# Kernel optimization log

Hardware: AMD Instinct MI355X
Metric: run time of the kernel (lower is better)

The kernel has to match this reference:

```python
import jax, jax.numpy as jnp
import numpy as np
import math

B, S, HID, NH = 2, 2048, 1024, 16
HD = HID // NH


def setup_inputs() -> dict:
    key = jax.random.key(0)
    ks = jax.random.split(key, 6)
    scale = 0.02
    return {
        "hidden_states": jax.random.normal(ks[0], (B, S, HID), dtype=jnp.float32),
        "attention_mask": jnp.ones((B, S), dtype=jnp.float32),
        "Wq": jax.random.normal(ks[1], (HID, HID), dtype=jnp.float32) * scale,
        "bq": jnp.zeros((HID,), dtype=jnp.float32),
        "Wk": jax.random.normal(ks[2], (HID, HID), dtype=jnp.float32) * scale,
        "bk": jnp.zeros((HID,), dtype=jnp.float32),
        "Wv": jax.random.normal(ks[3], (HID, HID), dtype=jnp.float32) * scale,
        "bv": jnp.zeros((HID,), dtype=jnp.float32),
        "Wo": jax.random.normal(ks[4], (HID, HID), dtype=jnp.float32) * scale,
        "bo": jnp.zeros((HID,), dtype=jnp.float32),
        "beta": jnp.zeros((1,), dtype=jnp.float32),
        "gamma": jnp.ones((1,), dtype=jnp.float32),
    }


def reference(hidden_states, attention_mask, Wq, bq, Wk, bk, Wv, bv, Wo, bo, beta, gamma):
    b, s, h = hidden_states.shape

    def proj(W, bias):
        # torch Linear: x @ W.T + b ; then split heads -> [B, NH, S, HD]
        y = jnp.einsum('bsh,oh->bso', hidden_states, W) + bias
        return y.reshape(b, s, NH, HD).transpose(0, 2, 1, 3)

    q = proj(Wq, bq)
    k = proj(Wk, bk)
    v = proj(Wv, bv)

    scores = jnp.einsum('bnsd,bntd->bnst', q, k) / math.sqrt(HD)  # [B,NH,S,S]
    # extended mask: [B,1,1,S]; additive -1e4 on masked positions
    scores = scores + (1.0 - attention_mask)[:, None, None, :] * (-10000.0)

    # ConsMax: exp(scores - beta - rowmax) / gamma (no sum normalization)
    shifted = scores - beta
    shifted = shifted - jnp.max(shifted, axis=-1, keepdims=True)
    probs = jnp.exp(shifted) / gamma  # dropout p=0 -> identity

    ctx = jnp.einsum('bnst,bntd->bnsd', probs, v)  # [B,NH,S,HD]
    ctx = ctx.transpose(0, 2, 1, 3).reshape(b, s, h)
    return jnp.einsum('bsh,oh->bso', ctx, Wo) + bo
```

## Files before the change

### kernel.cpp

```cpp
#include <hip/hip_runtime.h>
#include <hip/hip_bf16.h>


typedef unsigned short u16;
typedef __attribute__((ext_vector_type(8))) short short8;
typedef __attribute__((ext_vector_type(4))) float floatx4;
typedef __attribute__((ext_vector_type(16))) float floatx16;

constexpr int B_  = 2;
constexpr int S_  = 2048;
constexpr int HID = 1024;
constexpr int NH  = 16;
constexpr int HD  = 64;

constexpr float LOG2E   = 1.4426950408889634f;
constexpr float QSCALE  = 0.125f * LOG2E;
constexpr float MSCALE  = -10000.0f * LOG2E;

#if __has_builtin(__builtin_amdgcn_exp2f)
#define EXP2(x) __builtin_amdgcn_exp2f(x)
#else
#define EXP2(x) exp2f(x)
#endif

__device__ __forceinline__ u16 f2us(float f) {
    union { float f; unsigned int i; } x;
    x.f = f;
    unsigned int r = x.i + 0x7FFFu + ((x.i >> 16) & 1u);
    return (u16)(r >> 16);
}
__device__ __forceinline__ unsigned pk2(float a, float b) {
    __hip_bfloat162 h = __float22bfloat162_rn(make_float2(a, b));
    unsigned u; __builtin_memcpy(&u, &h, 4); return u;
}
__device__ __forceinline__ void async_lds16(const u16* g, u16* l) {
    __builtin_amdgcn_global_load_lds(
        (const __attribute__((address_space(1))) unsigned int*)g,
        (__attribute__((address_space(3))) unsigned int*)l, 16, 0, 0);
}

__global__ __launch_bounds__(256)
void cvt_all(const float* __restrict__ hs, const float* __restrict__ Wq,
             const float* __restrict__ Wk, const float* __restrict__ Wv,
             const float* __restrict__ Wo,
             u16* __restrict__ hs_bf, u16* __restrict__ Wcat,
             u16* __restrict__ Wo_bf)
{
    const int bid = blockIdx.x;
    const float* src;
    u16* dst;
    size_t base;
    if (bid < 4096) {
        src = hs; dst = hs_bf; base = (size_t)bid * 1024;
    } else if (bid < 7168) {
        const int s = (bid - 4096) >> 10;
        src = (s == 0) ? Wq : (s == 1) ? Wk : Wv;
        dst = Wcat + (size_t)s * 1048576;
        base = (size_t)((bid - 4096) & 1023) * 1024;
    } else {
        src = Wo; dst = Wo_bf; base = (size_t)(bid - 7168) * 1024;
    }
    const size_t i = base + threadIdx.x * 4;
    float4 t = *(const float4*)(src + i);
    uint2 o = { pk2(t.x, t.y), pk2(t.z, t.w) };
    *(uint2*)(dst + i) = o;
}

__global__ __launch_bounds__(256)
void qkv_gemm(const u16* __restrict__ hs_bf, const u16* __restrict__ Wcat,
              const float* __restrict__ bq, const float* __restrict__ bk,
              const float* __restrict__ bv,
              u16* __restrict__ Qo, u16* __restrict__ Ko, u16* __restrict__ VT)
{
    __shared__ u16 Alds[3][4096];
    __shared__ u16 Blds[3][4096];

    const int tid = threadIdx.x;
    const int id  = blockIdx.x;
    const int xcd = id & 7, jb = id >> 3;
    const int m0  = (xcd * 4 + (jb & 3)) * 128;
    const int n0g = (jb >> 2) * 128;
    const int p   = n0g >> 10;
    const int n0  = n0g & 1023;
    const u16*   Wb = Wcat + (size_t)p * 1048576;
    const float* bi = (p == 0) ? bq : (p == 1) ? bk : bv;
    const float  osc = (p == 0) ? QSCALE : 1.0f;

    const int w = tid >> 6, l = tid & 63;
    const int quad = l >> 4, l16 = l & 15;
    const int wy = w >> 1, wx = w & 1;

    floatx4 acc[4][4];
    #pragma unroll
    for (int i = 0; i < 4; ++i)
        #pragma unroll
        for (int j = 0; j < 4; ++j) acc[i][j] = (floatx4){0.f, 0.f, 0.f, 0.f};

    auto stage = [&](int ks, int bf) {
        const int k0 = ks * 32;
        #pragma unroll
        for (int c = 0; c < 2; ++c) {
            const int s = w * 2 + c;
            async_lds16(hs_bf + (size_t)(m0 + s * 16 + l16) * HID + k0 + quad * 8,
                        &Alds[bf][s * 512]);
            async_lds16(Wb + (size_t)(n0 + s * 16 + l16) * HID + k0 + quad * 8,
                        &Blds[bf][s * 512]);
        }
    };

    constexpr int NS = HID / 32;
    stage(0, 0);
    stage(1, 1);

    for (int ks = 0; ks < NS; ++ks) {
        const int cur = ks % 3;
        if (ks < NS - 1) asm volatile("s_waitcnt vmcnt(4)" ::: "memory");
        else             asm volatile("s_waitcnt vmcnt(0)" ::: "memory");
        __builtin_amdgcn_s_barrier();
        if (ks + 2 < NS) stage(ks + 2, (ks + 2) % 3);

        short8 afr[4], bfr[4];
        #pragma unroll
        for (int i = 0; i < 4; ++i)
            afr[i] = *(const short8*)&Alds[cur][(wy * 4 + i) * 512 + l * 8];
        #pragma unroll
        for (int j = 0; j < 4; ++j)
            bfr[j] = *(const short8*)&Blds[cur][(wx * 4 + j) * 512 + l * 8];
        #pragma unroll
        for (int i = 0; i < 4; ++i)
            #pragma unroll
            for (int j = 0; j < 4; ++j)
                acc[i][j] = __builtin_amdgcn_mfma_f32_16x16x32_bf16(afr[i], bfr[j], acc[i][j], 0, 0, 0);
    }

    #pragma unroll
    for (int i = 0; i < 4; ++i)
        #pragma unroll
        for (int j = 0; j < 4; ++j) {
            const int nn   = n0 + wx * 64 + j * 16 + l16;
            const int head = nn >> 6, dd = nn & 63;
            const float bb_ = bi[nn];
            const int mmb = m0 + wy * 64 + i * 16 + quad * 4;
            const int b = mmb >> 11, ss = mmb & (S_ - 1);
            if (p == 2) {
                uint2 st = { pk2(acc[i][j][0] + bb_, acc[i][j][1] + bb_),
                             pk2(acc[i][j][2] + bb_, acc[i][j][3] + bb_) };
                *(uint2*)(VT + (((size_t)(b * NH + head)) * HD + dd) * S_ + ss) = st;
            } else {
                u16* Out = (p == 0) ? Qo : Ko;
                #pragma unroll
                for (int rg = 0; rg < 4; ++rg)
                    Out[(((size_t)b * NH + head) * S_ + ss + rg) * HD + dd] =
                        f2us((acc[i][j][rg] + bb_) * osc);
            }
        }
}

__global__ __launch_bounds__(512, 4)
void attn13(const u16* __restrict__ Qg, const u16* __restrict__ Kg,
            const u16* __restrict__ VTg, const float* __restrict__ mask,
            const float* __restrict__ gamma, u16* __restrict__ ctx)
{
    __shared__ u16 SMEM[36864];
    u16*   KbB = SMEM;
    u16*   VbB = SMEM + 12288;
    u16*   PqB = SMEM + 24576;
    float* Mb  = (float*)(SMEM + 32768);

    const int tid = threadIdx.x;
    const int w = tid >> 6, l = tid & 63;
    const int wq = w & 3, wk = w >> 2;
    const int l32 = l & 31, hh = l >> 5;
    const int swz = (l32 & 3) << 3;
    const int id  = blockIdx.x;
    const int xcd = id & 7, jb = id >> 3;
    const int bh  = xcd * 4 + (jb >> 4);
    const int qb  = jb & 15;
    const int b0  = bh >> 4, h = bh & (NH - 1);

    const u16* Qb    = Qg  + (size_t)bh * S_ * HD;
    const u16* Kbg   = Kg  + (size_t)bh * S_ * HD;
    const u16* Vbg   = VTg + (size_t)bh * HD * S_;
    const float* mG  = mask + (size_t)b0 * S_;

    const int qrow = qb * 128 + wq * 32 + l32;

    short8 qB[4];
    #pragma unroll
    for (int dc = 0; dc < 4; ++dc)
        qB[dc] = *(const short8*)(Qb + (size_t)qrow * HD + dc * 16 + hh * 8);

    {
        float4 mv = *(const float4*)(mG + tid * 4);
        float* d = &Mb[tid * 4];
        d[0] = fmaf(mv.x, -MSCALE, MSCALE);
        d[1] = fmaf(mv.y, -MSCALE, MSCALE);
        d[2] = fmaf(mv.z, -MSCALE, MSCALE);
        d[3] = fmaf(mv.w, -MSCALE, MSCALE);
    }

    floatx16 oacc[2];
    #pragma unroll
    for (int db = 0; db < 2; ++db)
        #pragma unroll
        for (int i = 0; i < 16; ++i) oacc[db][i] = 0.f;
    float m_run = -1e30f;

    u16* Kbuf = KbB + wk * 6144;
    u16* Vbuf = VbB + wk * 6144;
    u16* Pw   = PqB + w * 1024;

    auto stage = [&](int i, int bf) {
        const int kt = 2 * i + wk;
        async_lds16(Kbg + (size_t)(kt * 32 + l32) * HD + wq * 16 + hh * 8,
                    Kbuf + bf * 2048 + wq * 512);
        const int db = wq >> 1, kg = wq & 1;
        async_lds16(Vbg + (size_t)(db * 32 + l32) * S_ + kt * 32 + kg * 16 + hh * 8,
                    Vbuf + bf * 2048 + wq * 512);
    };

    __syncthreads();
    constexpr int NI = 32;
    stage(0, 0);
    stage(1, 1);

    for (int i = 0; i < NI; ++i) {
        const int cur = i % 3;
        if (i < NI - 1) asm volatile("s_waitcnt vmcnt(2)" ::: "memory");
        else            asm volatile("s_waitcnt vmcnt(0)" ::: "memory");
        __builtin_amdgcn_s_barrier();
        if (i + 2 < NI) stage(i + 2, (i + 2) % 3);

        const int kt = 2 * i + wk;

        const float* mrow = &Mb[kt * 32 + 4 * hh];
        floatx16 acc;
        #pragma unroll
        for (int g = 0; g < 4; ++g) {
            float4 mv = *(const float4*)(mrow + g * 8);
            acc[4*g]   = mv.x;
            acc[4*g+1] = mv.y;
            acc[4*g+2] = mv.z;
            acc[4*g+3] = mv.w;
        }
        #pragma unroll
        for (int dc = 0; dc < 4; ++dc) {
            short8 kf = *(const short8*)&Kbuf[cur * 2048 + dc * 512 + l * 8];
            acc = __builtin_amdgcn_mfma_f32_32x32x16_bf16(kf, qB[dc], acc, 0, 0, 0);
        }

        float mr = m_run;
        #pragma unroll
        for (int ii = 0; ii < 16; ++ii) mr = fmaxf(mr, acc[ii]);
        m_run = mr;
        #pragma unroll
        for (int g = 0; g < 4; ++g) {
            uint2 pw = { pk2(EXP2(acc[4*g]),   EXP2(acc[4*g+1])),
                         pk2(EXP2(acc[4*g+2]), EXP2(acc[4*g+3])) };
            const int koff = 8 * g + 4 * hh;
            *(uint2*)&Pw[l32 * 32 + (koff ^ swz)] = pw;
        }

        #pragma unroll
        for (int kg = 0; kg < 2; ++kg) {
            short8 pf = *(const short8*)&Pw[l32 * 32 + ((kg * 16 + hh * 8) ^ swz)];
            #pragma unroll
            for (int db = 0; db < 2; ++db) {
                short8 vf = *(const short8*)&Vbuf[cur * 2048 + (db * 2 + kg) * 512 + l * 8];
                oacc[db] = __builtin_amdgcn_mfma_f32_32x32x16_bf16(vf, pf, oacc[db], 0, 0, 0);
            }
        }
    }

    __syncthreads();
    float* OS = (float*)SMEM;
    if (wk == 1) {
        float* d = OS + (size_t)(wq * 64 + l) * 33;
        #pragma unroll
        for (int db = 0; db < 2; ++db)
            #pragma unroll
            for (int ii = 0; ii < 16; ++ii) d[db * 16 + ii] = oacc[db][ii];
        d[32] = m_run;
    }
    __syncthreads();
    if (wk == 0) {
        const float* s = OS + (size_t)(wq * 64 + l) * 33;
        #pragma unroll
        for (int db = 0; db < 2; ++db)
            #pragma unroll
            for (int ii = 0; ii < 16; ++ii) oacc[db][ii] += s[db * 16 + ii];
        m_run = fmaxf(m_run, s[32]);
        const float mx = fmaxf(m_run, __shfl_xor(m_run, 32, 64));
        const float si = EXP2(-mx) * (1.0f / gamma[0]);
        u16* crow = ctx + (size_t)(b0 * S_ + qrow) * HID + h * HD;
        #pragma unroll
        for (int db = 0; db < 2; ++db)
            #pragma unroll
            for (int g = 0; g < 4; ++g) {
                uint2 st = { pk2(oacc[db][g * 4 + 0] * si, oacc[db][g * 4 + 1] * si),
                             pk2(oacc[db][g * 4 + 2] * si, oacc[db][g * 4 + 3] * si) };
                *(uint2*)(crow + db * 32 + g * 8 + hh * 4) = st;
            }
    }
}

__global__ __launch_bounds__(256)
void out_gemm(const u16* __restrict__ ctx, const u16* __restrict__ Wo_bf,
              const float* __restrict__ bo, float* __restrict__ out)
{
    __shared__ u16 Alds[3][4096];
    __shared__ u16 Blds[3][2048];

    const int tid = threadIdx.x;
    const int id  = blockIdx.x;
    const int xcd = id & 7, jb = id >> 3;
    const int m0  = (xcd * 4 + (jb & 3)) * 128;
    const int n0  = (jb >> 2) * 64;

    const int w = tid >> 6, l = tid & 63;
    const int quad = l >> 4, l16 = l & 15;

    floatx4 acc[2][4];
    #pragma unroll
    for (int i = 0; i < 2; ++i)
        #pragma unroll
        for (int j = 0; j < 4; ++j) acc[i][j] = (floatx4){0.f, 0.f, 0.f, 0.f};

    auto stage = [&](int ks, int bf) {
        const int k0 = ks * 32;
        #pragma unroll
        for (int c = 0; c < 2; ++c) {
            const int s = w * 2 + c;
            async_lds16(ctx + (size_t)(m0 + s * 16 + l16) * HID + k0 + quad * 8,
                        &Alds[bf][s * 512]);
        }
        async_lds16(Wo_bf + (size_t)(n0 + w * 16 + l16) * HID + k0 + quad * 8,
                    &Blds[bf][w * 512]);
    };

    constexpr int NS = HID / 32;
    stage(0, 0);
    stage(1, 1);

    for (int ks = 0; ks < NS; ++ks) {
        const int cur = ks % 3;
        if (ks < NS - 1) asm volatile("s_waitcnt vmcnt(3)" ::: "memory");
        else             asm volatile("s_waitcnt vmcnt(0)" ::: "memory");
        __builtin_amdgcn_s_barrier();
        if (ks + 2 < NS) stage(ks + 2, (ks + 2) % 3);

        short8 afr[2], bfr[4];
        #pragma unroll
        for (int i = 0; i < 2; ++i)
            afr[i] = *(const short8*)&Alds[cur][(w * 2 + i) * 512 + l * 8];
        #pragma unroll
        for (int j = 0; j < 4; ++j)
            bfr[j] = *(const short8*)&Blds[cur][j * 512 + l * 8];
        #pragma unroll
        for (int i = 0; i < 2; ++i)
            #pragma unroll
            for (int j = 0; j < 4; ++j)
                acc[i][j] = __builtin_amdgcn_mfma_f32_16x16x32_bf16(afr[i], bfr[j], acc[i][j], 0, 0, 0);
    }

    #pragma unroll
    for (int i = 0; i < 2; ++i)
        #pragma unroll
        for (int j = 0; j < 4; ++j) {
            const int nn = n0 + j * 16 + l16;
            const float bb_ = bo[nn];
            #pragma unroll
            for (int rg = 0; rg < 4; ++rg) {
                const int mm = m0 + w * 32 + i * 16 + quad * 4 + rg;
                out[(size_t)mm * HID + nn] = acc[i][j][rg] + bb_;
            }
        }
}

extern "C" void kernel_launch(void* const* d_in, const int* in_sizes, int n_in,
                              void* d_out, int out_size, void* d_ws, size_t ws_size,
                              hipStream_t stream)
{
    const float* hs    = (const float*)d_in[0];
    const float* mask  = (const float*)d_in[1];
    const float* Wq    = (const float*)d_in[2];
    const float* bq    = (const float*)d_in[3];
    const float* Wk    = (const float*)d_in[4];
    const float* bk    = (const float*)d_in[5];
    const float* Wv    = (const float*)d_in[6];
    const float* bv    = (const float*)d_in[7];
    const float* Wo    = (const float*)d_in[8];
    const float* bo    = (const float*)d_in[9];
    const float* gamma = (const float*)d_in[11];
    float* out = (float*)d_out;

    const size_t tsz = (size_t)B_ * NH * S_ * HD;
    u16* q     = (u16*)d_ws;
    u16* vT    = q + tsz;
    u16* Wcat  = vT + tsz;
    u16* Wo_bf = Wcat + 3u * 1048576u;
    u16* ctx   = Wo_bf + 1048576u;
    u16* hs_bf = (u16*)d_out;
    u16* kbuf  = hs_bf + tsz;

    cvt_all<<<dim3(8192), 256, 0, stream>>>(hs, Wq, Wk, Wv, Wo, hs_bf, Wcat, Wo_bf);
    qkv_gemm<<<dim3(768), 256, 0, stream>>>(hs_bf, Wcat, bq, bk, bv, q, kbuf, vT);
    attn13<<<dim3(512), 512, 0, stream>>>(q, kbuf, vT, mask, gamma, ctx);
    out_gemm<<<dim3(512), 256, 0, stream>>>(ctx, Wo_bf, bo, out);
}
```

Baseline: 233.9 us.

## Load K/V directly into registers with double-buffered prefetch, dropping LDS staging

The attention kernel no longer stages K and V tiles through shared memory with async copies and per-iteration barriers. Each wave now loads its own K/V fragments straight from global memory into two register sets, alternating between them across 64-key tiles, which removes the block-wide barrier from the inner loop. The P tile is widened to 64 keys and its swizzle extended to match. The cost is far higher register pressure, since the launch-bounds occupancy hint was dropped and 32 short8 values are held live. Waves also stop sharing K/V loads, so global or L2 traffic rises.

After: 296.6 us. 1.27x slower.

```diff
diff --git a/kernel.cpp b/kernel.cpp
--- a/kernel.cpp
+++ b/kernel.cpp
@@ -156,22 +156,20 @@
         }
 }
 
-__global__ __launch_bounds__(512, 4)
-void attn13(const u16* __restrict__ Qg, const u16* __restrict__ Kg,
+__global__ __launch_bounds__(512)
+void attn14(const u16* __restrict__ Qg, const u16* __restrict__ Kg,
             const u16* __restrict__ VTg, const float* __restrict__ mask,
             const float* __restrict__ gamma, u16* __restrict__ ctx)
 {
-    __shared__ u16 SMEM[36864];
-    u16*   KbB = SMEM;
-    u16*   VbB = SMEM + 12288;
-    u16*   PqB = SMEM + 24576;
-    float* Mb  = (float*)(SMEM + 32768);
+    __shared__ u16 SMEM[20480];
+    u16*   PqB = SMEM;
+    float* Mb  = (float*)(SMEM + 16384);
 
     const int tid = threadIdx.x;
     const int w = tid >> 6, l = tid & 63;
     const int wq = w & 3, wk = w >> 2;
     const int l32 = l & 31, hh = l >> 5;
-    const int swz = (l32 & 3) << 3;
+    const int swz = (l32 & 7) << 3;
     const int id  = blockIdx.x;
     const int xcd = id & 7, jb = id >> 3;
     const int bh  = xcd * 4 + (jb >> 4);
@@ -198,6 +196,7 @@
         d[2] = fmaf(mv.z, -MSCALE, MSCALE);
         d[3] = fmaf(mv.w, -MSCALE, MSCALE);
     }
+    __syncthreads();
 
     floatx16 oacc[2];
     #pragma unroll
@@ -206,71 +205,65 @@
         for (int i = 0; i < 16; ++i) oacc[db][i] = 0.f;
     float m_run = -1e30f;
 
-    u16* Kbuf = KbB + wk * 6144;
-    u16* Vbuf = VbB + wk * 6144;
-    u16* Pw   = PqB + w * 1024;
-
-    auto stage = [&](int i, int bf) {
-        const int kt = 2 * i + wk;
-        async_lds16(Kbg + (size_t)(kt * 32 + l32) * HD + wq * 16 + hh * 8,
-                    Kbuf + bf * 2048 + wq * 512);
-        const int db = wq >> 1, kg = wq & 1;
-        async_lds16(Vbg + (size_t)(db * 32 + l32) * S_ + kt * 32 + kg * 16 + hh * 8,
-                    Vbuf + bf * 2048 + wq * 512);
-    };
-
-    __syncthreads();
-    constexpr int NI = 32;
-    stage(0, 0);
-    stage(1, 1);
-
-    for (int i = 0; i < NI; ++i) {
-        const int cur = i % 3;
-        if (i < NI - 1) asm volatile("s_waitcnt vmcnt(2)" ::: "memory");
-        else            asm volatile("s_waitcnt vmcnt(0)" ::: "memory");
-        __builtin_amdgcn_s_barrier();
-        if (i + 2 < NI) stage(i + 2, (i + 2) % 3);
-
-        const int kt = 2 * i + wk;
-
-        const float* mrow = &Mb[kt * 32 + 4 * hh];
-        floatx16 acc;
-        #pragma unroll
-        for (int g = 0; g < 4; ++g) {
-            float4 mv = *(const float4*)(mrow + g * 8);
-            acc[4*g]   = mv.x;
-            acc[4*g+1] = mv.y;
-            acc[4*g+2] = mv.z;
-            acc[4*g+3] = mv.w;
-        }
-        #pragma unroll
-        for (int dc = 0; dc < 4; ++dc) {
-            short8 kf = *(const short8*)&Kbuf[cur * 2048 + dc * 512 + l * 8];
-            acc = __builtin_amdgcn_mfma_f32_32x32x16_bf16(kf, qB[dc], acc, 0, 0, 0);
-        }
-
-        float mr = m_run;
-        #pragma unroll
-        for (int ii = 0; ii < 16; ++ii) mr = fmaxf(mr, acc[ii]);
-        m_run = mr;
-        #pragma unroll
-        for (int g = 0; g < 4; ++g) {
-            uint2 pw = { pk2(EXP2(acc[4*g]),   EXP2(acc[4*g+1])),
-                         pk2(EXP2(acc[4*g+2]), EXP2(acc[4*g+3])) };
-            const int koff = 8 * g + 4 * hh;
-            *(uint2*)&Pw[l32 * 32 + (koff ^ swz)] = pw;
-        }
-
-        #pragma unroll
-        for (int kg = 0; kg < 2; ++kg) {
-            short8 pf = *(const short8*)&Pw[l32 * 32 + ((kg * 16 + hh * 8) ^ swz)];
-            #pragma unroll
-            for (int db = 0; db < 2; ++db) {
-                short8 vf = *(const short8*)&Vbuf[cur * 2048 + (db * 2 + kg) * 512 + l * 8];
-                oacc[db] = __builtin_amdgcn_mfma_f32_32x32x16_bf16(vf, pf, oacc[db], 0, 0, 0);
-            }
-        }
-    }
+    u16* Pw = PqB + w * 2048;
+
+    struct KV { short8 k[8]; short8 v[8]; };
+    KV A, B;
+
+#define LOADKV(D, KT) do {                                                     \
+    const int _kt = (KT);                                                      \
+    _Pragma("unroll") for (int _hb = 0; _hb < 2; ++_hb)                        \
+        _Pragma("unroll") for (int _dc = 0; _dc < 4; ++_dc)                    \
+            D.k[_hb*4+_dc] = *(const short8*)(Kbg +                            \
+                (size_t)(_kt*64 + _hb*32 + l32)*HD + _dc*16 + hh*8);           \
+    _Pragma("unroll") for (int _db = 0; _db < 2; ++_db)                        \
+        _Pragma("unroll") for (int _kg = 0; _kg < 4; ++_kg)                    \
+            D.v[_db*4+_kg] = *(const short8*)(Vbg +                            \
+                (size_t)(_db*32 + l32)*S_ + _kt*64 + _kg*16 + hh*8);           \
+} while (0)
+
+#define COMPUTE(Sb, KT) do {                                                   \
+    const int _kt = (KT);                                                      \
+    _Pragma("unroll") for (int _hb = 0; _hb < 2; ++_hb) {                      \
+        const float* _mrow = &Mb[_kt*64 + _hb*32 + 4*hh];                      \
+        floatx16 _acc;                                                         \
+        _Pragma("unroll") for (int _g = 0; _g < 4; ++_g) {                     \
+            float4 _mv = *(const float4*)(_mrow + _g*8);                       \
+            _acc[4*_g]   = _mv.x; _acc[4*_g+1] = _mv.y;                        \
+            _acc[4*_g+2] = _mv.z; _acc[4*_g+3] = _mv.w;                        \
+        }                                                                      \
+        _Pragma("unroll") for (int _dc = 0; _dc < 4; ++_dc)                    \
+            _acc = __builtin_amdgcn_mfma_f32_32x32x16_bf16(                    \
+                Sb.k[_hb*4+_dc], qB[_dc], _acc, 0, 0, 0);                      \
+        float _mr = m_run;                                                     \
+        _Pragma("unroll") for (int _ii = 0; _ii < 16; ++_ii)                   \
+            _mr = fmaxf(_mr, _acc[_ii]);                                       \
+        m_run = _mr;                                                           \
+        _Pragma("unroll") for (int _g = 0; _g < 4; ++_g) {                     \
+            uint2 _pw = { pk2(EXP2(_acc[4*_g]),   EXP2(_acc[4*_g+1])),         \
+                          pk2(EXP2(_acc[4*_g+2]), EXP2(_acc[4*_g+3])) };       \
+            const int _koff = _hb*32 + 8*_g + 4*hh;                            \
+            *(uint2*)&Pw[l32*64 + (_koff ^ swz)] = _pw;                        \
+        }                                                                      \
+    }                                                                          \
+    _Pragma("unroll") for (int _kg = 0; _kg < 4; ++_kg) {                      \
+        short8 _pf = *(const short8*)&Pw[l32*64 + ((_kg*16 + hh*8) ^ swz)];    \
+        _Pragma("unroll") for (int _db = 0; _db < 2; ++_db)                    \
+            oacc[_db] = __builtin_amdgcn_mfma_f32_32x32x16_bf16(               \
+                Sb.v[_db*4+_kg], _pf, oacc[_db], 0, 0, 0);                     \
+    }                                                                          \
+} while (0)
+
+    LOADKV(A, wk);
+    #pragma unroll
+    for (int jj = 0; jj < 8; ++jj) {
+        LOADKV(B, 2 * (2 * jj + 1) + wk);
+        COMPUTE(A, 2 * (2 * jj) + wk);
+        if (jj < 7) LOADKV(A, 2 * (2 * jj + 2) + wk);
+        COMPUTE(B, 2 * (2 * jj + 1) + wk);
+    }
+#undef LOADKV
+#undef COMPUTE
 
     __syncthreads();
     float* OS = (float*)SMEM;
@@ -405,6 +398,6 @@
 
     cvt_all<<<dim3(8192), 256, 0, stream>>>(hs, Wq, Wk, Wv, Wo, hs_bf, Wcat, Wo_bf);
     qkv_gemm<<<dim3(768), 256, 0, stream>>>(hs_bf, Wcat, bq, bk, bv, q, kbuf, vT);
-    attn13<<<dim3(512), 512, 0, stream>>>(q, kbuf, vT, mask, gamma, ctx);
+    attn14<<<dim3(512), 512, 0, stream>>>(q, kbuf, vT, mask, gamma, ctx);
     out_gemm<<<dim3(512), 256, 0, stream>>>(ctx, Wo_bf, bo, out);
 }
```
